# Optimization experiments

Measured on AMD Instinct MI355X. Metric: run time of the kernel, lower is better.

## Reference

```python
import jax, jax.numpy as jnp
import numpy as np

INV_TEMPERATURE = 0.125  # 1/sqrt(head_dim=64)

B, P, H, I, J, D = 2, 64, 8, 256, 256, 64


def setup_inputs() -> dict:
    key = jax.random.key(0)
    k1, k2, k3, k4 = jax.random.split(key, 4)
    q = jax.random.normal(k1, (B, P, H, I, D), dtype=jnp.float32)
    k = jax.random.normal(k2, (B, P, H, J, D), dtype=jnp.float32)
    v = jax.random.normal(k3, (B, P, H, J, D), dtype=jnp.float32)
    pos_scores = jax.random.normal(k4, (B, P, H, I, J), dtype=jnp.float32)
    mask = jnp.ones((B, P, H, I, J), dtype=jnp.float32)
    return {"q": q, "k": k, "v": v, "pos_scores": pos_scores, "mask": mask}


def reference(q, k, v, pos_scores, mask):
    # windowed QK^T: [b,p,h,i,d] x [b,p,h,j,d] -> [b,p,h,i,j]
    sim = jnp.einsum('bphid,bphjd->bphij', q, k) * INV_TEMPERATURE
    sim = sim + pos_scores          # additive positional bias
    sim = mask * sim                # multiplicative mask (as in original)
    attn = jax.nn.softmax(sim, axis=-1)
    out = jnp.einsum('bphij,bphjd->bphid', attn, v)
    return out
```

## Files before the change

kernel.cpp:

```cpp
#include <hip/hip_runtime.h>


typedef short short8 __attribute__((ext_vector_type(8)));
typedef float f32x4 __attribute__((ext_vector_type(4)));
typedef int int4v __attribute__((ext_vector_type(4)));

__device__ __forceinline__ unsigned bf16r(float x) {
  unsigned u = __float_as_uint(x);
  return (u + 0x7FFFu + ((u >> 16) & 1u)) >> 16;
}
__device__ __forceinline__ unsigned pk(float a, float b) {
  return bf16r(a) | (bf16r(b) << 16);
}
__device__ __forceinline__ short8 pack8(float4 a, float4 b) {
  int4v t;
  t[0] = (int)pk(a.x, a.y); t[1] = (int)pk(a.z, a.w);
  t[2] = (int)pk(b.x, b.y); t[3] = (int)pk(b.z, b.w);
  return __builtin_bit_cast(short8, t);
}

__global__ __launch_bounds__(512, 2)
void WindowedMaskedAttentionCalculation_72189810311255_kernel(
    const float* __restrict__ q, const float* __restrict__ k,
    const float* __restrict__ v, const float* __restrict__ pos,
    const float* __restrict__ msk, float* __restrict__ out) {
  __shared__ unsigned short Kb[16384];
  __shared__ unsigned short Vt[16384];

  const int s = blockIdx.x;
  const int tid = threadIdx.x;
  const size_t qkvOff = (size_t)s * 16384;
  const size_t pmOff = (size_t)s * 65536;

  const float4* K4 = (const float4*)(k + qkvOff);
  const float4* V4 = (const float4*)(v + qkvOff);
#pragma unroll
  for (int it = 0; it < 8; ++it) {
    int f4 = it * 512 + tid;
    int j = f4 >> 4;
    int c4 = f4 & 15;
    float4 kv = K4[f4];
    unsigned lo = pk(kv.x, kv.y), hi = pk(kv.z, kv.w);
    int gs = (c4 >> 1) ^ (j & 7);
    *(uint2*)&Kb[j * 64 + gs * 8 + (c4 & 1) * 4] = make_uint2(lo, hi);

    float4 vv = V4[f4];
    float vals[4] = {vv.x, vv.y, vv.z, vv.w};
    int dc = c4 * 4;
#pragma unroll
    for (int c = 0; c < 4; ++c) {
      int d = dc + c;
      int gv = (j >> 3) ^ (d & 15);
      Vt[d * 256 + gv * 8 + (j & 7)] = (unsigned short)bf16r(vals[c]);
    }
  }
  __syncthreads();

  const int w = tid >> 6, l = tid & 63, g = l >> 4, il = l & 15;
  const float* Qs = q + qkvOff;
  const float4* Pos4 = (const float4*)(pos + pmOff);
  const float4* Msk4 = (const float4*)(msk + pmOff);
  float* Out = out + qkvOff;
  const f32x4 zero = {0.f, 0.f, 0.f, 0.f};

#pragma unroll 1
  for (int chunk = 0; chunk < 2; ++chunk) {
    const int i0 = (w * 2 + chunk) * 16;
    const int irow = i0 + il;

    const float4* Qr = (const float4*)(Qs + (size_t)irow * 64);
    short8 qf0 = pack8(Qr[2 * g], Qr[2 * g + 1]);
    short8 qf1 = pack8(Qr[8 + 2 * g], Qr[9 + 2 * g]);

    float sv[16][4];
#pragma unroll
    for (int jt = 0; jt < 16; ++jt) {
      float4 pf = Pos4[(size_t)irow * 64 + jt * 4 + g];
      float4 mf = Msk4[(size_t)irow * 64 + jt * 4 + g];
      int j16 = jt * 16 + il;
      const short8* kr = (const short8*)&Kb[j16 * 64];
      short8 kf0 = kr[(0 + g) ^ (j16 & 7)];
      short8 kf1 = kr[(4 + g) ^ (j16 & 7)];
      f32x4 acc = __builtin_amdgcn_mfma_f32_16x16x32_bf16(kf0, qf0, zero, 0, 0, 0);
      acc = __builtin_amdgcn_mfma_f32_16x16x32_bf16(kf1, qf1, acc, 0, 0, 0);
      sv[jt][0] = (acc[0] * 0.125f + pf.x) * mf.x;
      sv[jt][1] = (acc[1] * 0.125f + pf.y) * mf.y;
      sv[jt][2] = (acc[2] * 0.125f + pf.z) * mf.z;
      sv[jt][3] = (acc[3] * 0.125f + pf.w) * mf.w;
    }

    float mx = -3.4e38f;
#pragma unroll
    for (int jt = 0; jt < 16; ++jt)
#pragma unroll
      for (int r = 0; r < 4; ++r) mx = fmaxf(mx, sv[jt][r]);
    mx = fmaxf(mx, __shfl_xor(mx, 16));
    mx = fmaxf(mx, __shfl_xor(mx, 32));
    float sum = 0.f;
#pragma unroll
    for (int jt = 0; jt < 16; ++jt)
#pragma unroll
      for (int r = 0; r < 4; ++r) {
        float e = exp2f((sv[jt][r] - mx) * 1.44269504088896340736f);
        sv[jt][r] = e;
        sum += e;
      }
    sum += __shfl_xor(sum, 16);
    sum += __shfl_xor(sum, 32);
    float rcp = 1.0f / sum;

    unsigned pd[16][2];
#pragma unroll
    for (int jt = 0; jt < 16; ++jt) {
      pd[jt][0] = pk(sv[jt][0], sv[jt][1]);
      pd[jt][1] = pk(sv[jt][2], sv[jt][3]);
    }

    f32x4 ao[4] = {zero, zero, zero, zero};
    const int addrA = (((g & 1) * 2) * 16 + il) * 4;
    const int addrB = addrA + 64;
    const bool hi = (g >> 1) != 0;
#pragma unroll
    for (int kt = 0; kt < 8; ++kt) {
      int t0 = 2 * kt, t1 = t0 + 1;
      int a0 = __builtin_amdgcn_ds_bpermute(addrA, (int)pd[t0][0]);
      int b0 = __builtin_amdgcn_ds_bpermute(addrA, (int)pd[t1][0]);
      int a1 = __builtin_amdgcn_ds_bpermute(addrA, (int)pd[t0][1]);
      int b1 = __builtin_amdgcn_ds_bpermute(addrA, (int)pd[t1][1]);
      int a2 = __builtin_amdgcn_ds_bpermute(addrB, (int)pd[t0][0]);
      int b2 = __builtin_amdgcn_ds_bpermute(addrB, (int)pd[t1][0]);
      int a3 = __builtin_amdgcn_ds_bpermute(addrB, (int)pd[t0][1]);
      int b3 = __builtin_amdgcn_ds_bpermute(addrB, (int)pd[t1][1]);
      int4v av;
      av[0] = hi ? b0 : a0;
      av[1] = hi ? b1 : a1;
      av[2] = hi ? b2 : a2;
      av[3] = hi ? b3 : a3;
      short8 af = __builtin_bit_cast(short8, av);
#pragma unroll
      for (int dt = 0; dt < 4; ++dt) {
        int d = dt * 16 + il;
        const short8* vr = (const short8*)&Vt[d * 256];
        short8 vf = vr[(4 * kt + g) ^ il];
        ao[dt] = __builtin_amdgcn_mfma_f32_16x16x32_bf16(af, vf, ao[dt], 0, 0, 0);
      }
    }

    float rl[4];
#pragma unroll
    for (int r = 0; r < 4; ++r) rl[r] = __shfl(rcp, g * 4 + r);
#pragma unroll
    for (int dt = 0; dt < 4; ++dt)
#pragma unroll
      for (int r = 0; r < 4; ++r)
        Out[(size_t)(i0 + g * 4 + r) * 64 + dt * 16 + il] = ao[dt][r] * rl[r];
  }
}

extern "C" void kernel_launch(void* const* d_in, const int* in_sizes, int n_in,
                              void* d_out, int out_size, void* d_ws, size_t ws_size,
                              hipStream_t stream) {
  const float* q = (const float*)d_in[0];
  const float* k = (const float*)d_in[1];
  const float* v = (const float*)d_in[2];
  const float* pos = (const float*)d_in[3];
  const float* msk = (const float*)d_in[4];
  float* out = (float*)d_out;
  WindowedMaskedAttentionCalculation_72189810311255_kernel<<<1024, 512, 0, stream>>>(
      q, k, v, pos, msk, out);
}
```

Measured before the change: 799.4 us.

## Convert attention to online softmax with double-buffered pos/mask prefetch

Replaces the two-pass softmax, which held all 64 scores per lane in registers, with an online softmax over 32-column tiles that interleaves QK, exp and PV MFMAs. It adds lazy rescaling that only fires when the running max grows by more than 8, and a two-deep register prefetch of pos_scores and mask. The aim is to cut register pressure and overlap global loads with compute. In exchange it adds per-tile cross-lane max reductions and wave-uniform branches, and when rescaling is skipped the unnormalised exponentials can reach up to e^8 before the bf16 packing.

```diff
diff --git a/kernel.cpp b/kernel.cpp
--- a/kernel.cpp
+++ b/kernel.cpp
@@ -18,6 +18,8 @@
   t[2] = (int)pk(b.x, b.y); t[3] = (int)pk(b.z, b.w);
   return __builtin_bit_cast(short8, t);
 }
+
+#define LOG2E 1.44269504088896340736f
 
 __global__ __launch_bounds__(512, 2)
 void WindowedMaskedAttentionCalculation_72189810311255_kernel(
@@ -63,6 +65,10 @@
   float* Out = out + qkvOff;
   const f32x4 zero = {0.f, 0.f, 0.f, 0.f};
 
+  const int addrA = (((g & 1) * 2) * 16 + il) * 4;
+  const int addrB = addrA + 64;
+  const bool hi = (g >> 1) != 0;
+
 #pragma unroll 1
   for (int chunk = 0; chunk < 2; ++chunk) {
     const int i0 = (w * 2 + chunk) * 16;
@@ -72,65 +78,89 @@
     short8 qf0 = pack8(Qr[2 * g], Qr[2 * g + 1]);
     short8 qf1 = pack8(Qr[8 + 2 * g], Qr[9 + 2 * g]);
 
-    float sv[16][4];
-#pragma unroll
-    for (int jt = 0; jt < 16; ++jt) {
-      float4 pf = Pos4[(size_t)irow * 64 + jt * 4 + g];
-      float4 mf = Msk4[(size_t)irow * 64 + jt * 4 + g];
-      int j16 = jt * 16 + il;
-      const short8* kr = (const short8*)&Kb[j16 * 64];
-      short8 kf0 = kr[(0 + g) ^ (j16 & 7)];
-      short8 kf1 = kr[(4 + g) ^ (j16 & 7)];
-      f32x4 acc = __builtin_amdgcn_mfma_f32_16x16x32_bf16(kf0, qf0, zero, 0, 0, 0);
-      acc = __builtin_amdgcn_mfma_f32_16x16x32_bf16(kf1, qf1, acc, 0, 0, 0);
-      sv[jt][0] = (acc[0] * 0.125f + pf.x) * mf.x;
-      sv[jt][1] = (acc[1] * 0.125f + pf.y) * mf.y;
-      sv[jt][2] = (acc[2] * 0.125f + pf.z) * mf.z;
-      sv[jt][3] = (acc[3] * 0.125f + pf.w) * mf.w;
+    float4 pfb[2][2], mfb[2][2];
+#pragma unroll
+    for (int t = 0; t < 2; ++t) {
+      pfb[t][0] = Pos4[(size_t)irow * 64 + (2 * t) * 4 + g];
+      mfb[t][0] = Msk4[(size_t)irow * 64 + (2 * t) * 4 + g];
+      pfb[t][1] = Pos4[(size_t)irow * 64 + (2 * t + 1) * 4 + g];
+      mfb[t][1] = Msk4[(size_t)irow * 64 + (2 * t + 1) * 4 + g];
     }
 
-    float mx = -3.4e38f;
-#pragma unroll
-    for (int jt = 0; jt < 16; ++jt)
-#pragma unroll
-      for (int r = 0; r < 4; ++r) mx = fmaxf(mx, sv[jt][r]);
-    mx = fmaxf(mx, __shfl_xor(mx, 16));
-    mx = fmaxf(mx, __shfl_xor(mx, 32));
-    float sum = 0.f;
-#pragma unroll
-    for (int jt = 0; jt < 16; ++jt)
+    f32x4 ao[4] = {zero, zero, zero, zero};
+    float m = -3.0e38f, lsum = 0.f;
+
+#pragma unroll
+    for (int t = 0; t < 8; ++t) {
+      float4 pf0 = pfb[t & 1][0], mf0 = mfb[t & 1][0];
+      float4 pf1 = pfb[t & 1][1], mf1 = mfb[t & 1][1];
+      if (t < 6) {
+        pfb[t & 1][0] = Pos4[(size_t)irow * 64 + (2 * (t + 2)) * 4 + g];
+        mfb[t & 1][0] = Msk4[(size_t)irow * 64 + (2 * (t + 2)) * 4 + g];
+        pfb[t & 1][1] = Pos4[(size_t)irow * 64 + (2 * (t + 2) + 1) * 4 + g];
+        mfb[t & 1][1] = Msk4[(size_t)irow * 64 + (2 * (t + 2) + 1) * 4 + g];
+      }
+
+      int j16a = (2 * t) * 16 + il;
+      const short8* kra = (const short8*)&Kb[j16a * 64];
+      short8 ka0 = kra[(0 + g) ^ (j16a & 7)];
+      short8 ka1 = kra[(4 + g) ^ (j16a & 7)];
+      f32x4 acc0 = __builtin_amdgcn_mfma_f32_16x16x32_bf16(ka0, qf0, zero, 0, 0, 0);
+      acc0 = __builtin_amdgcn_mfma_f32_16x16x32_bf16(ka1, qf1, acc0, 0, 0, 0);
+      int j16b = (2 * t + 1) * 16 + il;
+      const short8* krb = (const short8*)&Kb[j16b * 64];
+      short8 kb0 = krb[(0 + g) ^ (j16b & 7)];
+      short8 kb1 = krb[(4 + g) ^ (j16b & 7)];
+      f32x4 acc1 = __builtin_amdgcn_mfma_f32_16x16x32_bf16(kb0, qf0, zero, 0, 0, 0);
+      acc1 = __builtin_amdgcn_mfma_f32_16x16x32_bf16(kb1, qf1, acc1, 0, 0, 0);
+
+      float s0[4], s1[4];
+      s0[0] = (acc0[0] * 0.125f + pf0.x) * mf0.x;
+      s0[1] = (acc0[1] * 0.125f + pf0.y) * mf0.y;
+      s0[2] = (acc0[2] * 0.125f + pf0.z) * mf0.z;
+      s0[3] = (acc0[3] * 0.125f + pf0.w) * mf0.w;
+      s1[0] = (acc1[0] * 0.125f + pf1.x) * mf1.x;
+      s1[1] = (acc1[1] * 0.125f + pf1.y) * mf1.y;
+      s1[2] = (acc1[2] * 0.125f + pf1.z) * mf1.z;
+      s1[3] = (acc1[3] * 0.125f + pf1.w) * mf1.w;
+
+      float tmax = fmaxf(fmaxf(fmaxf(s0[0], s0[1]), fmaxf(s0[2], s0[3])),
+                         fmaxf(fmaxf(s1[0], s1[1]), fmaxf(s1[2], s1[3])));
+      tmax = fmaxf(tmax, __shfl_xor(tmax, 16));
+      tmax = fmaxf(tmax, __shfl_xor(tmax, 32));
+
+      if (__any(tmax > m + 8.0f)) {
+        float nm = fmaxf(m, tmax);
+        float sc = exp2f((m - nm) * LOG2E);
+        float scr[4];
+#pragma unroll
+        for (int r = 0; r < 4; ++r) scr[r] = __shfl(sc, g * 4 + r);
+#pragma unroll
+        for (int dt = 0; dt < 4; ++dt)
+#pragma unroll
+          for (int r = 0; r < 4; ++r) ao[dt][r] *= scr[r];
+        lsum *= sc;
+        m = nm;
+      }
+
+      float p0[4], p1[4];
 #pragma unroll
       for (int r = 0; r < 4; ++r) {
-        float e = exp2f((sv[jt][r] - mx) * 1.44269504088896340736f);
-        sv[jt][r] = e;
-        sum += e;
-      }
-    sum += __shfl_xor(sum, 16);
-    sum += __shfl_xor(sum, 32);
-    float rcp = 1.0f / sum;
-
-    unsigned pd[16][2];
-#pragma unroll
-    for (int jt = 0; jt < 16; ++jt) {
-      pd[jt][0] = pk(sv[jt][0], sv[jt][1]);
-      pd[jt][1] = pk(sv[jt][2], sv[jt][3]);
-    }
-
-    f32x4 ao[4] = {zero, zero, zero, zero};
-    const int addrA = (((g & 1) * 2) * 16 + il) * 4;
-    const int addrB = addrA + 64;
-    const bool hi = (g >> 1) != 0;
-#pragma unroll
-    for (int kt = 0; kt < 8; ++kt) {
-      int t0 = 2 * kt, t1 = t0 + 1;
-      int a0 = __builtin_amdgcn_ds_bpermute(addrA, (int)pd[t0][0]);
-      int b0 = __builtin_amdgcn_ds_bpermute(addrA, (int)pd[t1][0]);
-      int a1 = __builtin_amdgcn_ds_bpermute(addrA, (int)pd[t0][1]);
-      int b1 = __builtin_amdgcn_ds_bpermute(addrA, (int)pd[t1][1]);
-      int a2 = __builtin_amdgcn_ds_bpermute(addrB, (int)pd[t0][0]);
-      int b2 = __builtin_amdgcn_ds_bpermute(addrB, (int)pd[t1][0]);
-      int a3 = __builtin_amdgcn_ds_bpermute(addrB, (int)pd[t0][1]);
-      int b3 = __builtin_amdgcn_ds_bpermute(addrB, (int)pd[t1][1]);
+        p0[r] = exp2f((s0[r] - m) * LOG2E);
+        p1[r] = exp2f((s1[r] - m) * LOG2E);
+        lsum += p0[r] + p1[r];
+      }
+      unsigned pd00 = pk(p0[0], p0[1]), pd01 = pk(p0[2], p0[3]);
+      unsigned pd10 = pk(p1[0], p1[1]), pd11 = pk(p1[2], p1[3]);
+
+      int a0 = __builtin_amdgcn_ds_bpermute(addrA, (int)pd00);
+      int b0 = __builtin_amdgcn_ds_bpermute(addrA, (int)pd10);
+      int a1 = __builtin_amdgcn_ds_bpermute(addrA, (int)pd01);
+      int b1 = __builtin_amdgcn_ds_bpermute(addrA, (int)pd11);
+      int a2 = __builtin_amdgcn_ds_bpermute(addrB, (int)pd00);
+      int b2 = __builtin_amdgcn_ds_bpermute(addrB, (int)pd10);
+      int a3 = __builtin_amdgcn_ds_bpermute(addrB, (int)pd01);
+      int b3 = __builtin_amdgcn_ds_bpermute(addrB, (int)pd11);
       int4v av;
       av[0] = hi ? b0 : a0;
       av[1] = hi ? b1 : a1;
@@ -141,11 +171,14 @@
       for (int dt = 0; dt < 4; ++dt) {
         int d = dt * 16 + il;
         const short8* vr = (const short8*)&Vt[d * 256];
-        short8 vf = vr[(4 * kt + g) ^ il];
+        short8 vf = vr[(4 * t + g) ^ il];
         ao[dt] = __builtin_amdgcn_mfma_f32_16x16x32_bf16(af, vf, ao[dt], 0, 0, 0);
       }
     }
 
+    lsum += __shfl_xor(lsum, 16);
+    lsum += __shfl_xor(lsum, 32);
+    float rcp = 1.0f / lsum;
     float rl[4];
 #pragma unroll
     for (int r = 0; r < 4; ++r) rl[r] = __shfl(rcp, g * 4 + r);
```

Measured after the change: 712.3 us. 1.12x faster.
